# Kernel optimization log

Measured on AMD Instinct MI355X. Metric: run time of the kernel, lower is better.

The kernel has to match this reference:

```python
import jax, jax.numpy as jnp
import numpy as np

N_NODES = 100000
N_EDGES = 3200000  # avg degree 32
D_IN = 128
D_OUT = 64
BN_EPS = 0.001


def setup_inputs() -> dict:
    key = jax.random.key(0)
    k1, k2, k3, k4, k5 = jax.random.split(key, 5)
    x = jax.random.normal(k1, (N_NODES, D_IN), dtype=jnp.float32)
    W = jax.random.normal(k2, (D_IN, D_OUT), dtype=jnp.float32) * 0.05
    edge_val = jax.random.uniform(k3, (N_EDGES,), dtype=jnp.float32)
    edge_src = jax.random.randint(k4, (N_EDGES,), 0, N_NODES, dtype=jnp.int32)
    edge_dst = jax.random.randint(k5, (N_EDGES,), 0, N_NODES, dtype=jnp.int32)
    return {"x": x, "W": W, "edge_val": edge_val,
            "edge_src": edge_src, "edge_dst": edge_dst}


def reference(x, W, edge_val, edge_src, edge_dst):
    # pre_sup = X @ W  (dense feature transform; dropout rate is 0 -> identity)
    pre_sup = x @ W  # [N, D_OUT]
    # support = A @ pre_sup, A given in COO form: A[dst, src] = edge_val
    msgs = edge_val[:, None] * pre_sup[edge_src]          # [E, D_OUT]
    out = jax.ops.segment_sum(msgs, edge_dst, num_segments=N_NODES)  # [N, D_OUT]
    # tf.nn.moments over all-but-last axis + batch_norm (no scale/offset, eps=1e-3)
    mean = jnp.mean(out, axis=0)
    var = jnp.var(out, axis=0)
    out = (out - mean) * jax.lax.rsqrt(var + BN_EPS)
    return jax.nn.relu(out)
```

## Files before the change

kernel.cpp:

```cpp
#include <hip/hip_runtime.h>
#include <stdint.h>

#define D_IN  128
#define D_OUT 64
#define BN_EPS 1e-3f

#define BIN_SHIFT 7
#define BIN_NODES 128
#define BIN_CAP   5120
#define CHUNK     8192
#define MAX_BINS  800
#define PT_STRIDE 72

typedef __attribute__((ext_vector_type(8))) short bf16x8;
typedef __attribute__((ext_vector_type(4))) float f32x4;

__device__ __forceinline__ ushort f32_to_bf16_rne(float f) {
  uint u = __float_as_uint(f);
  u += 0x7FFFu + ((u >> 16) & 1u);
  return (ushort)(u >> 16);
}
__device__ __forceinline__ float bf16_to_f32(ushort h) {
  return __uint_as_float((uint)h << 16);
}

__global__ __launch_bounds__(256) void gemm_mfma_kernel(
    const float* __restrict__ x, const float* __restrict__ W,
    ushort* __restrict__ pre16, int* __restrict__ bin_cursor,
    float* __restrict__ stats, int n_bins, int n_nodes, int n_tiles) {
  __shared__ ushort Wb[D_IN * D_OUT];
  __shared__ ushort ptile[64 * PT_STRIDE];
  const int t = threadIdx.x;
  if (blockIdx.x == 0) {
    for (int i = t; i < n_bins; i += 256) bin_cursor[i] = 0;
    if (t < 128) stats[t] = 0.f;
  }
  for (int i = t; i < D_IN * D_OUT; i += 256) Wb[i] = f32_to_bf16_rne(W[i]);
  __syncthreads();

  const int lane = t & 63;
  const int wave = t >> 6;
  const int m = lane & 15;
  const int quad = lane >> 4;

  bf16x8 bfrag[4][4];
#pragma unroll
  for (int nt = 0; nt < 4; ++nt)
#pragma unroll
    for (int s = 0; s < 4; ++s)
#pragma unroll
      for (int j = 0; j < 8; ++j)
        bfrag[nt][s][j] =
            (short)Wb[(32 * s + quad * 8 + j) * D_OUT + nt * 16 + m];

  for (int tile = blockIdx.x; tile < n_tiles; tile += gridDim.x) {
    const int rbase0 = tile * 64;
    const int row = rbase0 + wave * 16 + m;
    const size_t rl = (size_t)min(row, n_nodes - 1);
    f32x4 acc0 = {0.f, 0.f, 0.f, 0.f}, acc1 = {0.f, 0.f, 0.f, 0.f};
    f32x4 acc2 = {0.f, 0.f, 0.f, 0.f}, acc3 = {0.f, 0.f, 0.f, 0.f};
#pragma unroll
    for (int s = 0; s < 4; ++s) {
      const float4 xa = *(const float4*)&x[rl * D_IN + s * 32 + quad * 8];
      const float4 xb = *(const float4*)&x[rl * D_IN + s * 32 + quad * 8 + 4];
      bf16x8 af;
      af[0] = (short)f32_to_bf16_rne(xa.x);
      af[1] = (short)f32_to_bf16_rne(xa.y);
      af[2] = (short)f32_to_bf16_rne(xa.z);
      af[3] = (short)f32_to_bf16_rne(xa.w);
      af[4] = (short)f32_to_bf16_rne(xb.x);
      af[5] = (short)f32_to_bf16_rne(xb.y);
      af[6] = (short)f32_to_bf16_rne(xb.z);
      af[7] = (short)f32_to_bf16_rne(xb.w);
      acc0 = __builtin_amdgcn_mfma_f32_16x16x32_bf16(af, bfrag[0][s], acc0, 0, 0, 0);
      acc1 = __builtin_amdgcn_mfma_f32_16x16x32_bf16(af, bfrag[1][s], acc1, 0, 0, 0);
      acc2 = __builtin_amdgcn_mfma_f32_16x16x32_bf16(af, bfrag[2][s], acc2, 0, 0, 0);
      acc3 = __builtin_amdgcn_mfma_f32_16x16x32_bf16(af, bfrag[3][s], acc3, 0, 0, 0);
    }
    __syncthreads();
#pragma unroll
    for (int reg = 0; reg < 4; ++reg) {
      const int lr = wave * 16 + quad * 4 + reg;
      ptile[lr * PT_STRIDE + m]      = f32_to_bf16_rne(acc0[reg]);
      ptile[lr * PT_STRIDE + 16 + m] = f32_to_bf16_rne(acc1[reg]);
      ptile[lr * PT_STRIDE + 32 + m] = f32_to_bf16_rne(acc2[reg]);
      ptile[lr * PT_STRIDE + 48 + m] = f32_to_bf16_rne(acc3[reg]);
    }
    __syncthreads();
    {
      const int lr = t >> 2;
      const int sg = t & 3;
      const int r = rbase0 + lr;
      if (r < n_nodes) {
        const uint4* pl = (const uint4*)&ptile[lr * PT_STRIDE + sg * 16];
        uint4* po = (uint4*)&pre16[(size_t)r * D_OUT + sg * 16];
        po[0] = pl[0];
        po[1] = pl[1];
      }
    }
  }
}

__global__ __launch_bounds__(256) void partition_kernel(
    const float* __restrict__ ev, const int* __restrict__ esrc,
    const int* __restrict__ edst, int* __restrict__ bin_cursor,
    uint2* __restrict__ bucket, int n_edges, int n_bins) {
  __shared__ int cnt[MAX_BINS];
  __shared__ int base[MAX_BINS];
  const int t = threadIdx.x;
  const int beg = blockIdx.x * CHUNK;
  const int end = min(beg + CHUNK, n_edges);

  for (int i = t; i < n_bins; i += 256) cnt[i] = 0;
  __syncthreads();

  for (int i = beg + t * 4; i < end; i += 1024) {
    if (i + 3 < end) {
      const int4 d4 = *(const int4*)&edst[i];
      atomicAdd(&cnt[d4.x >> BIN_SHIFT], 1);
      atomicAdd(&cnt[d4.y >> BIN_SHIFT], 1);
      atomicAdd(&cnt[d4.z >> BIN_SHIFT], 1);
      atomicAdd(&cnt[d4.w >> BIN_SHIFT], 1);
    } else {
      for (int k = i; k < end; ++k) atomicAdd(&cnt[edst[k] >> BIN_SHIFT], 1);
    }
  }
  __syncthreads();

  for (int i = t; i < n_bins; i += 256) {
    const int c = cnt[i];
    int b = 0;
    if (c > 0) b = atomicAdd(&bin_cursor[i], c);
    if (b > BIN_CAP) b = BIN_CAP;
    base[i] = i * BIN_CAP + b;
    cnt[i] = 0;
  }
  __syncthreads();

  for (int i = beg + t * 4; i < end; i += 1024) {
    if (i + 3 < end) {
      const int4 d4 = *(const int4*)&edst[i];
      const int4 s4 = *(const int4*)&esrc[i];
      const float4 v4 = *(const float4*)&ev[i];
#pragma unroll
      for (int k = 0; k < 4; ++k) {
        const int dst = (&d4.x)[k];
        const int src = (&s4.x)[k];
        const float v = (&v4.x)[k];
        const int bin = dst >> BIN_SHIFT;
        const int r = atomicAdd(&cnt[bin], 1);
        const int pos = base[bin] + r;
        if (pos < (bin + 1) * BIN_CAP) {
          const uint w0 = ((uint)(dst & (BIN_NODES - 1)) << 17) | (uint)src;
          bucket[pos] = make_uint2(w0, __float_as_uint(v));
        }
      }
    } else {
      for (int k = i; k < end; ++k) {
        const int dst = edst[k];
        const int bin = dst >> BIN_SHIFT;
        const int r = atomicAdd(&cnt[bin], 1);
        const int pos = base[bin] + r;
        if (pos < (bin + 1) * BIN_CAP) {
          const uint w0 = ((uint)(dst & (BIN_NODES - 1)) << 17) | (uint)esrc[k];
          bucket[pos] = make_uint2(w0, __float_as_uint(ev[k]));
        }
      }
    }
  }
}

__global__ __launch_bounds__(512) void bin_sort_gather_kernel(
    const ushort* __restrict__ pre16, const uint2* __restrict__ bucket,
    const int* __restrict__ bin_cursor, float* __restrict__ out,
    float* __restrict__ stats, int n_nodes) {
  __shared__ uint s_src[BIN_CAP];
  __shared__ ushort s_val[BIN_CAP];
  __shared__ int s_hist[BIN_NODES];
  __shared__ int s_off[BIN_NODES + 1];
  __shared__ int s_cur[BIN_NODES];

  const int t = threadIdx.x;
  const int bin = blockIdx.x;
  const int cnt = min(bin_cursor[bin], BIN_CAP);
  const int64_t rbase = (int64_t)bin * BIN_CAP;

  if (t < BIN_NODES) s_hist[t] = 0;
  __syncthreads();

  for (int i = t; i < cnt; i += 512)
    atomicAdd(&s_hist[bucket[rbase + i].x >> 17], 1);
  __syncthreads();

  int own = (t < BIN_NODES) ? s_hist[t] : 0;
  for (int off = 1; off < BIN_NODES; off <<= 1) {
    int u = 0;
    if (t < BIN_NODES && t >= off) u = s_hist[t - off];
    __syncthreads();
    if (t < BIN_NODES) s_hist[t] += u;
    __syncthreads();
  }
  if (t < BIN_NODES) {
    const int e = s_hist[t] - own;
    s_off[t] = e;
    s_cur[t] = e;
  }
  if (t == 0) s_off[BIN_NODES] = cnt;
  __syncthreads();

  for (int i = t; i < cnt; i += 512) {
    const uint2 r = bucket[rbase + i];
    const int d = r.x >> 17;
    const int p = atomicAdd(&s_cur[d], 1);
    s_src[p] = r.x & 0x1FFFFu;
    s_val[p] = f32_to_bf16_rne(__uint_as_float(r.y));
  }
  __syncthreads();

  const int lane = t & 63;
  const int wave = t >> 6;
  const int half = lane >> 5;
  const int hl = lane & 31;
  const int node0 = bin * BIN_NODES;
  float csx = 0.f, csy = 0.f, cs2x = 0.f, cs2y = 0.f;

  for (int nl = wave; nl < BIN_NODES; nl += 8) {
    const int node = node0 + nl;
    if (node < n_nodes) {
      const int jb = s_off[nl], je = s_off[nl + 1];
      float a0x = 0.f, a0y = 0.f, a1x = 0.f, a1y = 0.f;
      float a2x = 0.f, a2y = 0.f, a3x = 0.f, a3y = 0.f;
      float a4x = 0.f, a4y = 0.f, a5x = 0.f, a5y = 0.f;
      float a6x = 0.f, a6y = 0.f, a7x = 0.f, a7y = 0.f;
      int j = jb + half;
      for (; j + 14 < je; j += 16) {
        const uint src0 = s_src[j],      src1 = s_src[j + 2];
        const uint src2 = s_src[j + 4],  src3 = s_src[j + 6];
        const uint src4 = s_src[j + 8],  src5 = s_src[j + 10];
        const uint src6 = s_src[j + 12], src7 = s_src[j + 14];
        const float v0 = bf16_to_f32(s_val[j]);
        const float v1 = bf16_to_f32(s_val[j + 2]);
        const float v2 = bf16_to_f32(s_val[j + 4]);
        const float v3 = bf16_to_f32(s_val[j + 6]);
        const float v4 = bf16_to_f32(s_val[j + 8]);
        const float v5 = bf16_to_f32(s_val[j + 10]);
        const float v6 = bf16_to_f32(s_val[j + 12]);
        const float v7 = bf16_to_f32(s_val[j + 14]);
        const uint p0 = *(const uint*)&pre16[(size_t)src0 * D_OUT + 2 * hl];
        const uint p1 = *(const uint*)&pre16[(size_t)src1 * D_OUT + 2 * hl];
        const uint p2 = *(const uint*)&pre16[(size_t)src2 * D_OUT + 2 * hl];
        const uint p3 = *(const uint*)&pre16[(size_t)src3 * D_OUT + 2 * hl];
        const uint p4 = *(const uint*)&pre16[(size_t)src4 * D_OUT + 2 * hl];
        const uint p5 = *(const uint*)&pre16[(size_t)src5 * D_OUT + 2 * hl];
        const uint p6 = *(const uint*)&pre16[(size_t)src6 * D_OUT + 2 * hl];
        const uint p7 = *(const uint*)&pre16[(size_t)src7 * D_OUT + 2 * hl];
        a0x += v0 * bf16_to_f32((ushort)(p0 & 0xFFFFu));
        a0y += v0 * bf16_to_f32((ushort)(p0 >> 16));
        a1x += v1 * bf16_to_f32((ushort)(p1 & 0xFFFFu));
        a1y += v1 * bf16_to_f32((ushort)(p1 >> 16));
        a2x += v2 * bf16_to_f32((ushort)(p2 & 0xFFFFu));
        a2y += v2 * bf16_to_f32((ushort)(p2 >> 16));
        a3x += v3 * bf16_to_f32((ushort)(p3 & 0xFFFFu));
        a3y += v3 * bf16_to_f32((ushort)(p3 >> 16));
        a4x += v4 * bf16_to_f32((ushort)(p4 & 0xFFFFu));
        a4y += v4 * bf16_to_f32((ushort)(p4 >> 16));
        a5x += v5 * bf16_to_f32((ushort)(p5 & 0xFFFFu));
        a5y += v5 * bf16_to_f32((ushort)(p5 >> 16));
        a6x += v6 * bf16_to_f32((ushort)(p6 & 0xFFFFu));
        a6y += v6 * bf16_to_f32((ushort)(p6 >> 16));
        a7x += v7 * bf16_to_f32((ushort)(p7 & 0xFFFFu));
        a7y += v7 * bf16_to_f32((ushort)(p7 >> 16));
      }
      for (; j + 6 < je; j += 8) {
        const uint src0 = s_src[j],     src1 = s_src[j + 2];
        const uint src2 = s_src[j + 4], src3 = s_src[j + 6];
        const float v0 = bf16_to_f32(s_val[j]);
        const float v1 = bf16_to_f32(s_val[j + 2]);
        const float v2 = bf16_to_f32(s_val[j + 4]);
        const float v3 = bf16_to_f32(s_val[j + 6]);
        const uint p0 = *(const uint*)&pre16[(size_t)src0 * D_OUT + 2 * hl];
        const uint p1 = *(const uint*)&pre16[(size_t)src1 * D_OUT + 2 * hl];
        const uint p2 = *(const uint*)&pre16[(size_t)src2 * D_OUT + 2 * hl];
        const uint p3 = *(const uint*)&pre16[(size_t)src3 * D_OUT + 2 * hl];
        a0x += v0 * bf16_to_f32((ushort)(p0 & 0xFFFFu));
        a0y += v0 * bf16_to_f32((ushort)(p0 >> 16));
        a1x += v1 * bf16_to_f32((ushort)(p1 & 0xFFFFu));
        a1y += v1 * bf16_to_f32((ushort)(p1 >> 16));
        a2x += v2 * bf16_to_f32((ushort)(p2 & 0xFFFFu));
        a2y += v2 * bf16_to_f32((ushort)(p2 >> 16));
        a3x += v3 * bf16_to_f32((ushort)(p3 & 0xFFFFu));
        a3y += v3 * bf16_to_f32((ushort)(p3 >> 16));
      }
      for (; j < je; j += 2) {
        const uint src = s_src[j];
        const float v = bf16_to_f32(s_val[j]);
        const uint p = *(const uint*)&pre16[(size_t)src * D_OUT + 2 * hl];
        a0x += v * bf16_to_f32((ushort)(p & 0xFFFFu));
        a0y += v * bf16_to_f32((ushort)(p >> 16));
      }
      float ax = ((a0x + a1x) + (a2x + a3x)) + ((a4x + a5x) + (a6x + a7x));
      float ay = ((a0y + a1y) + (a2y + a3y)) + ((a4y + a5y) + (a6y + a7y));
      ax += __shfl_xor(ax, 32);
      ay += __shfl_xor(ay, 32);
      if (half == 0) {
        *(float2*)&out[(size_t)node * D_OUT + 2 * hl] = make_float2(ax, ay);
        csx += ax;
        cs2x += ax * ax;
        csy += ay;
        cs2y += ay * ay;
      }
    }
  }
  __syncthreads();

  float* red = (float*)s_src;
  float* red2 = red + 512;
  if (half == 0) {
    red[wave * 64 + 2 * hl] = csx;
    red[wave * 64 + 2 * hl + 1] = csy;
    red2[wave * 64 + 2 * hl] = cs2x;
    red2[wave * 64 + 2 * hl + 1] = cs2y;
  }
  __syncthreads();
  if (t < 64) {
    float s = 0.f, s2 = 0.f;
#pragma unroll
    for (int wv = 0; wv < 8; ++wv) {
      s += red[wv * 64 + t];
      s2 += red2[wv * 64 + t];
    }
    atomicAdd(&stats[t], s);
    atomicAdd(&stats[64 + t], s2);
  }
}

__global__ __launch_bounds__(256) void norm_kernel(
    float* __restrict__ out, const float* __restrict__ stats, int64_t n_vec4,
    float inv_n) {
  const int c = (threadIdx.x * 4) & 63;
  float mean[4], scale[4];
#pragma unroll
  for (int k = 0; k < 4; ++k) {
    mean[k] = stats[c + k] * inv_n;
    const float var = stats[64 + c + k] * inv_n - mean[k] * mean[k];
    scale[k] = rsqrtf(var + BN_EPS);
  }
  const int64_t stride = (int64_t)gridDim.x * 256;
  for (int64_t i = (int64_t)blockIdx.x * 256 + threadIdx.x; i < n_vec4;
       i += stride) {
    float4 v = ((float4*)out)[i];
    v.x = (v.x - mean[0]) * scale[0];
    v.y = (v.y - mean[1]) * scale[1];
    v.z = (v.z - mean[2]) * scale[2];
    v.w = (v.w - mean[3]) * scale[3];
    v.x = v.x > 0.f ? v.x : 0.f;
    v.y = v.y > 0.f ? v.y : 0.f;
    v.z = v.z > 0.f ? v.z : 0.f;
    v.w = v.w > 0.f ? v.w : 0.f;
    ((float4*)out)[i] = v;
  }
}

extern "C" void kernel_launch(void* const* d_in, const int* in_sizes, int n_in,
                              void* d_out, int out_size, void* d_ws,
                              size_t ws_size, hipStream_t stream) {
  const float* x = (const float*)d_in[0];
  const float* W = (const float*)d_in[1];
  const float* ev = (const float*)d_in[2];
  const int* esrc = (const int*)d_in[3];
  const int* edst = (const int*)d_in[4];

  const int n_nodes = in_sizes[0] / D_IN;
  const int n_edges = in_sizes[2];
  const int64_t n_out = (int64_t)n_nodes * D_OUT;
  const int n_bins = (n_nodes + BIN_NODES - 1) >> BIN_SHIFT;
  const int n_row_tiles = (n_nodes + 63) / 64;

  float* out = (float*)d_out;

  char* w = (char*)d_ws;
  ushort* pre16 = (ushort*)w;             w += (size_t)n_nodes * D_OUT * 2;
  int* bin_cursor = (int*)w;              w += (size_t)n_bins * 4;
  float* stats = (float*)w;               w += 128 * 4;
  w = (char*)(((uintptr_t)w + 7) & ~(uintptr_t)7);
  uint2* bucket = (uint2*)w;

  gemm_mfma_kernel<<<(n_row_tiles + 1) / 2, 256, 0, stream>>>(
      x, W, pre16, bin_cursor, stats, n_bins, n_nodes, n_row_tiles);
  partition_kernel<<<(n_edges + CHUNK - 1) / CHUNK, 256, 0, stream>>>(
      ev, esrc, edst, bin_cursor, bucket, n_edges, n_bins);
  bin_sort_gather_kernel<<<n_bins, 512, 0, stream>>>(pre16, bucket, bin_cursor,
                                                     out, stats, n_nodes);
  norm_kernel<<<2048, 256, 0, stream>>>(out, stats, n_out / 4,
                                        1.0f / (float)n_nodes);
}
```

Baseline: 292.6 us.

## Replace global bin atomics with per-chunk local bin offsets

```diff
diff --git a/kernel.cpp b/kernel.cpp
--- a/kernel.cpp
+++ b/kernel.cpp
@@ -10,6 +10,8 @@
 #define BIN_CAP   5120
 #define CHUNK     8192
 #define MAX_BINS  800
+#define LOFF_STRIDE 800
+#define MAX_CHUNKS 400
 #define PT_STRIDE 72
 
 typedef __attribute__((ext_vector_type(8))) short bf16x8;
@@ -26,15 +28,12 @@
 
 __global__ __launch_bounds__(256) void gemm_mfma_kernel(
     const float* __restrict__ x, const float* __restrict__ W,
-    ushort* __restrict__ pre16, int* __restrict__ bin_cursor,
-    float* __restrict__ stats, int n_bins, int n_nodes, int n_tiles) {
+    ushort* __restrict__ pre16, float* __restrict__ stats,
+    int n_nodes, int n_tiles) {
   __shared__ ushort Wb[D_IN * D_OUT];
   __shared__ ushort ptile[64 * PT_STRIDE];
   const int t = threadIdx.x;
-  if (blockIdx.x == 0) {
-    for (int i = t; i < n_bins; i += 256) bin_cursor[i] = 0;
-    if (t < 128) stats[t] = 0.f;
-  }
+  if (blockIdx.x == 0 && t < 128) stats[t] = 0.f;
   for (int i = t; i < D_IN * D_OUT; i += 256) Wb[i] = f32_to_bf16_rne(W[i]);
   __syncthreads();
 
@@ -103,10 +102,11 @@
 
 __global__ __launch_bounds__(256) void partition_kernel(
     const float* __restrict__ ev, const int* __restrict__ esrc,
-    const int* __restrict__ edst, int* __restrict__ bin_cursor,
+    const int* __restrict__ edst, int* __restrict__ loff_g,
     uint2* __restrict__ bucket, int n_edges, int n_bins) {
   __shared__ int cnt[MAX_BINS];
-  __shared__ int base[MAX_BINS];
+  __shared__ int loffs[MAX_BINS + 1];
+  __shared__ int sdata[256];
   const int t = threadIdx.x;
   const int beg = blockIdx.x * CHUNK;
   const int end = min(beg + CHUNK, n_edges);
@@ -127,15 +127,37 @@
   }
   __syncthreads();
 
-  for (int i = t; i < n_bins; i += 256) {
-    const int c = cnt[i];
-    int b = 0;
-    if (c > 0) b = atomicAdd(&bin_cursor[i], c);
-    if (b > BIN_CAP) b = BIN_CAP;
-    base[i] = i * BIN_CAP + b;
-    cnt[i] = 0;
-  }
-  __syncthreads();
+  {
+    const int b4 = t * 4;
+    int d0 = 0, d1 = 0, d2 = 0, d3 = 0;
+    if (b4 + 0 < n_bins) d0 = cnt[b4 + 0];
+    if (b4 + 1 < n_bins) d1 = cnt[b4 + 1];
+    if (b4 + 2 < n_bins) d2 = cnt[b4 + 2];
+    if (b4 + 3 < n_bins) d3 = cnt[b4 + 3];
+    const int s = d0 + d1 + d2 + d3;
+    sdata[t] = s;
+    __syncthreads();
+    for (int off = 1; off < 256; off <<= 1) {
+      const int u = (t >= off) ? sdata[t - off] : 0;
+      __syncthreads();
+      sdata[t] += u;
+      __syncthreads();
+    }
+    int run = sdata[t] - s;
+    if (b4 + 0 <= n_bins) loffs[b4 + 0] = run;  run += d0;
+    if (b4 + 1 <= n_bins) loffs[b4 + 1] = run;  run += d1;
+    if (b4 + 2 <= n_bins) loffs[b4 + 2] = run;  run += d2;
+    if (b4 + 3 <= n_bins) loffs[b4 + 3] = run;
+    if (b4 + 0 < n_bins) cnt[b4 + 0] = 0;
+    if (b4 + 1 < n_bins) cnt[b4 + 1] = 0;
+    if (b4 + 2 < n_bins) cnt[b4 + 2] = 0;
+    if (b4 + 3 < n_bins) cnt[b4 + 3] = 0;
+    if (t == 255) loffs[n_bins] = sdata[255];
+  }
+  __syncthreads();
+
+  for (int i = t; i <= n_bins; i += 256)
+    loff_g[blockIdx.x * LOFF_STRIDE + i] = loffs[i];
 
   for (int i = beg + t * 4; i < end; i += 1024) {
     if (i + 3 < end) {
@@ -145,26 +167,20 @@
 #pragma unroll
       for (int k = 0; k < 4; ++k) {
         const int dst = (&d4.x)[k];
-        const int src = (&s4.x)[k];
-        const float v = (&v4.x)[k];
         const int bin = dst >> BIN_SHIFT;
         const int r = atomicAdd(&cnt[bin], 1);
-        const int pos = base[bin] + r;
-        if (pos < (bin + 1) * BIN_CAP) {
-          const uint w0 = ((uint)(dst & (BIN_NODES - 1)) << 17) | (uint)src;
-          bucket[pos] = make_uint2(w0, __float_as_uint(v));
-        }
+        const uint w0 =
+            ((uint)(dst & (BIN_NODES - 1)) << 17) | (uint)(&s4.x)[k];
+        bucket[beg + loffs[bin] + r] =
+            make_uint2(w0, __float_as_uint((&v4.x)[k]));
       }
     } else {
       for (int k = i; k < end; ++k) {
         const int dst = edst[k];
         const int bin = dst >> BIN_SHIFT;
         const int r = atomicAdd(&cnt[bin], 1);
-        const int pos = base[bin] + r;
-        if (pos < (bin + 1) * BIN_CAP) {
-          const uint w0 = ((uint)(dst & (BIN_NODES - 1)) << 17) | (uint)esrc[k];
-          bucket[pos] = make_uint2(w0, __float_as_uint(ev[k]));
-        }
+        const uint w0 = ((uint)(dst & (BIN_NODES - 1)) << 17) | (uint)esrc[k];
+        bucket[beg + loffs[bin] + r] = make_uint2(w0, __float_as_uint(ev[k]));
       }
     }
   }
@@ -172,24 +188,34 @@
 
 __global__ __launch_bounds__(512) void bin_sort_gather_kernel(
     const ushort* __restrict__ pre16, const uint2* __restrict__ bucket,
-    const int* __restrict__ bin_cursor, float* __restrict__ out,
-    float* __restrict__ stats, int n_nodes) {
+    const int* __restrict__ loff_g, float* __restrict__ out,
+    float* __restrict__ stats, int n_nodes, int n_chunks, int n_bins) {
   __shared__ uint s_src[BIN_CAP];
   __shared__ ushort s_val[BIN_CAP];
   __shared__ int s_hist[BIN_NODES];
   __shared__ int s_off[BIN_NODES + 1];
   __shared__ int s_cur[BIN_NODES];
+  __shared__ int s_rs[MAX_CHUNKS];
+  __shared__ int s_re[MAX_CHUNKS];
 
   const int t = threadIdx.x;
   const int bin = blockIdx.x;
-  const int cnt = min(bin_cursor[bin], BIN_CAP);
-  const int64_t rbase = (int64_t)bin * BIN_CAP;
-
+
+  for (int r = t; r < n_chunks; r += 512) {
+    const int o0 = loff_g[r * LOFF_STRIDE + bin];
+    const int o1 = loff_g[r * LOFF_STRIDE + bin + 1];
+    s_rs[r] = r * CHUNK + o0;
+    s_re[r] = r * CHUNK + o1;
+  }
   if (t < BIN_NODES) s_hist[t] = 0;
   __syncthreads();
 
-  for (int i = t; i < cnt; i += 512)
-    atomicAdd(&s_hist[bucket[rbase + i].x >> 17], 1);
+  const int g16 = t >> 4;
+  const int l16 = t & 15;
+
+  for (int rr = g16; rr < n_chunks; rr += 32)
+    for (int i = s_rs[rr] + l16; i < s_re[rr]; i += 16)
+      atomicAdd(&s_hist[bucket[i].x >> 17], 1);
   __syncthreads();
 
   int own = (t < BIN_NODES) ? s_hist[t] : 0;
@@ -205,16 +231,19 @@
     s_off[t] = e;
     s_cur[t] = e;
   }
-  if (t == 0) s_off[BIN_NODES] = cnt;
-  __syncthreads();
-
-  for (int i = t; i < cnt; i += 512) {
-    const uint2 r = bucket[rbase + i];
-    const int d = r.x >> 17;
-    const int p = atomicAdd(&s_cur[d], 1);
-    s_src[p] = r.x & 0x1FFFFu;
-    s_val[p] = f32_to_bf16_rne(__uint_as_float(r.y));
-  }
+  if (t == 0) s_off[BIN_NODES] = s_hist[BIN_NODES - 1];
+  __syncthreads();
+
+  for (int rr = g16; rr < n_chunks; rr += 32)
+    for (int i = s_rs[rr] + l16; i < s_re[rr]; i += 16) {
+      const uint2 r = bucket[i];
+      const int d = r.x >> 17;
+      const int p = atomicAdd(&s_cur[d], 1);
+      if (p < BIN_CAP) {
+        s_src[p] = r.x & 0x1FFFFu;
+        s_val[p] = f32_to_bf16_rne(__uint_as_float(r.y));
+      }
+    }
   __syncthreads();
 
   const int lane = t & 63;
@@ -227,7 +256,8 @@
   for (int nl = wave; nl < BIN_NODES; nl += 8) {
     const int node = node0 + nl;
     if (node < n_nodes) {
-      const int jb = s_off[nl], je = s_off[nl + 1];
+      const int jb = min(s_off[nl], BIN_CAP);
+      const int je = min(s_off[nl + 1], BIN_CAP);
       float a0x = 0.f, a0y = 0.f, a1x = 0.f, a1y = 0.f;
       float a2x = 0.f, a2y = 0.f, a3x = 0.f, a3y = 0.f;
       float a4x = 0.f, a4y = 0.f, a5x = 0.f, a5y = 0.f;
@@ -375,22 +405,23 @@
   const int64_t n_out = (int64_t)n_nodes * D_OUT;
   const int n_bins = (n_nodes + BIN_NODES - 1) >> BIN_SHIFT;
   const int n_row_tiles = (n_nodes + 63) / 64;
+  const int n_chunks = (n_edges + CHUNK - 1) / CHUNK;
 
   float* out = (float*)d_out;
 
   char* w = (char*)d_ws;
   ushort* pre16 = (ushort*)w;             w += (size_t)n_nodes * D_OUT * 2;
-  int* bin_cursor = (int*)w;              w += (size_t)n_bins * 4;
   float* stats = (float*)w;               w += 128 * 4;
+  int* loff_g = (int*)w;                  w += (size_t)n_chunks * LOFF_STRIDE * 4;
   w = (char*)(((uintptr_t)w + 7) & ~(uintptr_t)7);
   uint2* bucket = (uint2*)w;
 
   gemm_mfma_kernel<<<(n_row_tiles + 1) / 2, 256, 0, stream>>>(
-      x, W, pre16, bin_cursor, stats, n_bins, n_nodes, n_row_tiles);
-  partition_kernel<<<(n_edges + CHUNK - 1) / CHUNK, 256, 0, stream>>>(
-      ev, esrc, edst, bin_cursor, bucket, n_edges, n_bins);
-  bin_sort_gather_kernel<<<n_bins, 512, 0, stream>>>(pre16, bucket, bin_cursor,
-                                                     out, stats, n_nodes);
+      x, W, pre16, stats, n_nodes, n_row_tiles);
+  partition_kernel<<<n_chunks, 256, 0, stream>>>(ev, esrc, edst, loff_g,
+                                                 bucket, n_edges, n_bins);
+  bin_sort_gather_kernel<<<n_bins, 512, 0, stream>>>(
+      pre16, bucket, loff_g, out, stats, n_nodes, n_chunks, n_bins);
   norm_kernel<<<2048, 256, 0, stream>>>(out, stats, n_out / 4,
                                         1.0f / (float)n_nodes);
 }
```

Result: no change. 293.4 us (+0.3%).

## Replace atomic bin cursor partition with histogram, scan, scatter passes

Applied to the files above, without the earlier changes.

```diff
diff --git a/kernel.cpp b/kernel.cpp
--- a/kernel.cpp
+++ b/kernel.cpp
@@ -10,6 +10,7 @@
 #define BIN_CAP   5120
 #define CHUNK     8192
 #define MAX_BINS  800
+#define LOFF_STRIDE 800
 #define PT_STRIDE 72
 
 typedef __attribute__((ext_vector_type(8))) short bf16x8;
@@ -26,15 +27,12 @@
 
 __global__ __launch_bounds__(256) void gemm_mfma_kernel(
     const float* __restrict__ x, const float* __restrict__ W,
-    ushort* __restrict__ pre16, int* __restrict__ bin_cursor,
-    float* __restrict__ stats, int n_bins, int n_nodes, int n_tiles) {
+    ushort* __restrict__ pre16, float* __restrict__ stats,
+    int n_nodes, int n_tiles) {
   __shared__ ushort Wb[D_IN * D_OUT];
   __shared__ ushort ptile[64 * PT_STRIDE];
   const int t = threadIdx.x;
-  if (blockIdx.x == 0) {
-    for (int i = t; i < n_bins; i += 256) bin_cursor[i] = 0;
-    if (t < 128) stats[t] = 0.f;
-  }
+  if (blockIdx.x == 0 && t < 128) stats[t] = 0.f;
   for (int i = t; i < D_IN * D_OUT; i += 256) Wb[i] = f32_to_bf16_rne(W[i]);
   __syncthreads();
 
@@ -101,20 +99,18 @@
   }
 }
 
-__global__ __launch_bounds__(256) void partition_kernel(
-    const float* __restrict__ ev, const int* __restrict__ esrc,
-    const int* __restrict__ edst, int* __restrict__ bin_cursor,
-    uint2* __restrict__ bucket, int n_edges, int n_bins) {
+__global__ __launch_bounds__(1024) void part_hist_kernel(
+    const int* __restrict__ edst, int* __restrict__ cnt_g, int n_edges,
+    int n_bins) {
   __shared__ int cnt[MAX_BINS];
-  __shared__ int base[MAX_BINS];
   const int t = threadIdx.x;
   const int beg = blockIdx.x * CHUNK;
   const int end = min(beg + CHUNK, n_edges);
 
-  for (int i = t; i < n_bins; i += 256) cnt[i] = 0;
-  __syncthreads();
-
-  for (int i = beg + t * 4; i < end; i += 1024) {
+  for (int i = t; i < n_bins; i += 1024) cnt[i] = 0;
+  __syncthreads();
+
+  for (int i = beg + t * 4; i < end; i += 4096) {
     if (i + 3 < end) {
       const int4 d4 = *(const int4*)&edst[i];
       atomicAdd(&cnt[d4.x >> BIN_SHIFT], 1);
@@ -127,17 +123,46 @@
   }
   __syncthreads();
 
-  for (int i = t; i < n_bins; i += 256) {
-    const int c = cnt[i];
-    int b = 0;
-    if (c > 0) b = atomicAdd(&bin_cursor[i], c);
-    if (b > BIN_CAP) b = BIN_CAP;
-    base[i] = i * BIN_CAP + b;
+  for (int i = t; i < n_bins; i += 1024)
+    cnt_g[blockIdx.x * LOFF_STRIDE + i] = cnt[i];
+}
+
+__global__ __launch_bounds__(512) void part_scan_kernel(
+    const int* __restrict__ cnt_g, int* __restrict__ goff,
+    int* __restrict__ bin_total, int n_chunks) {
+  __shared__ int sdata[512];
+  const int b = blockIdx.x;
+  const int t = threadIdx.x;
+  const int v = (t < n_chunks) ? cnt_g[t * LOFF_STRIDE + b] : 0;
+  sdata[t] = v;
+  __syncthreads();
+  for (int off = 1; off < 512; off <<= 1) {
+    const int u = (t >= off) ? sdata[t - off] : 0;
+    __syncthreads();
+    sdata[t] += u;
+    __syncthreads();
+  }
+  if (t < n_chunks) goff[t * LOFF_STRIDE + b] = sdata[t] - v;
+  if (t == n_chunks - 1) bin_total[b] = min(sdata[t], BIN_CAP);
+}
+
+__global__ __launch_bounds__(1024) void part_scatter_kernel(
+    const float* __restrict__ ev, const int* __restrict__ esrc,
+    const int* __restrict__ edst, const int* __restrict__ goff,
+    uint2* __restrict__ bucket, int n_edges, int n_bins) {
+  __shared__ int cnt[MAX_BINS];
+  __shared__ int base[MAX_BINS];
+  const int t = threadIdx.x;
+  const int beg = blockIdx.x * CHUNK;
+  const int end = min(beg + CHUNK, n_edges);
+
+  for (int i = t; i < n_bins; i += 1024) {
     cnt[i] = 0;
-  }
-  __syncthreads();
-
-  for (int i = beg + t * 4; i < end; i += 1024) {
+    base[i] = i * BIN_CAP + goff[blockIdx.x * LOFF_STRIDE + i];
+  }
+  __syncthreads();
+
+  for (int i = beg + t * 4; i < end; i += 4096) {
     if (i + 3 < end) {
       const int4 d4 = *(const int4*)&edst[i];
       const int4 s4 = *(const int4*)&esrc[i];
@@ -145,14 +170,13 @@
 #pragma unroll
       for (int k = 0; k < 4; ++k) {
         const int dst = (&d4.x)[k];
-        const int src = (&s4.x)[k];
-        const float v = (&v4.x)[k];
         const int bin = dst >> BIN_SHIFT;
         const int r = atomicAdd(&cnt[bin], 1);
         const int pos = base[bin] + r;
         if (pos < (bin + 1) * BIN_CAP) {
-          const uint w0 = ((uint)(dst & (BIN_NODES - 1)) << 17) | (uint)src;
-          bucket[pos] = make_uint2(w0, __float_as_uint(v));
+          const uint w0 =
+              ((uint)(dst & (BIN_NODES - 1)) << 17) | (uint)(&s4.x)[k];
+          bucket[pos] = make_uint2(w0, __float_as_uint((&v4.x)[k]));
         }
       }
     } else {
@@ -172,7 +196,7 @@
 
 __global__ __launch_bounds__(512) void bin_sort_gather_kernel(
     const ushort* __restrict__ pre16, const uint2* __restrict__ bucket,
-    const int* __restrict__ bin_cursor, float* __restrict__ out,
+    const int* __restrict__ bin_total, float* __restrict__ out,
     float* __restrict__ stats, int n_nodes) {
   __shared__ uint s_src[BIN_CAP];
   __shared__ ushort s_val[BIN_CAP];
@@ -182,7 +206,7 @@
 
   const int t = threadIdx.x;
   const int bin = blockIdx.x;
-  const int cnt = min(bin_cursor[bin], BIN_CAP);
+  const int cnt = bin_total[bin];
   const int64_t rbase = (int64_t)bin * BIN_CAP;
 
   if (t < BIN_NODES) s_hist[t] = 0;
@@ -375,21 +399,28 @@
   const int64_t n_out = (int64_t)n_nodes * D_OUT;
   const int n_bins = (n_nodes + BIN_NODES - 1) >> BIN_SHIFT;
   const int n_row_tiles = (n_nodes + 63) / 64;
+  const int n_chunks = (n_edges + CHUNK - 1) / CHUNK;
 
   float* out = (float*)d_out;
 
   char* w = (char*)d_ws;
   ushort* pre16 = (ushort*)w;             w += (size_t)n_nodes * D_OUT * 2;
-  int* bin_cursor = (int*)w;              w += (size_t)n_bins * 4;
   float* stats = (float*)w;               w += 128 * 4;
+  int* cnt_g = (int*)w;                   w += (size_t)n_chunks * LOFF_STRIDE * 4;
+  int* goff = (int*)w;                    w += (size_t)n_chunks * LOFF_STRIDE * 4;
+  int* bin_total = (int*)w;               w += (size_t)n_bins * 4;
   w = (char*)(((uintptr_t)w + 7) & ~(uintptr_t)7);
   uint2* bucket = (uint2*)w;
 
-  gemm_mfma_kernel<<<(n_row_tiles + 1) / 2, 256, 0, stream>>>(
-      x, W, pre16, bin_cursor, stats, n_bins, n_nodes, n_row_tiles);
-  partition_kernel<<<(n_edges + CHUNK - 1) / CHUNK, 256, 0, stream>>>(
-      ev, esrc, edst, bin_cursor, bucket, n_edges, n_bins);
-  bin_sort_gather_kernel<<<n_bins, 512, 0, stream>>>(pre16, bucket, bin_cursor,
+  gemm_mfma_kernel<<<n_row_tiles, 256, 0, stream>>>(
+      x, W, pre16, stats, n_nodes, n_row_tiles);
+  part_hist_kernel<<<n_chunks, 1024, 0, stream>>>(edst, cnt_g, n_edges,
+                                                  n_bins);
+  part_scan_kernel<<<n_bins, 512, 0, stream>>>(cnt_g, goff, bin_total,
+                                               n_chunks);
+  part_scatter_kernel<<<n_chunks, 1024, 0, stream>>>(ev, esrc, edst, goff,
+                                                     bucket, n_edges, n_bins);
+  bin_sort_gather_kernel<<<n_bins, 512, 0, stream>>>(pre16, bucket, bin_total,
                                                      out, stats, n_nodes);
   norm_kernel<<<2048, 256, 0, stream>>>(out, stats, n_out / 4,
                                         1.0f / (float)n_nodes);
```

Result: faster. 281.6 us (-3.8%).
